# Kernel optimization log

Measured on AMD Instinct MI355X. Metric: run time of the kernel, lower is better.

Reference implementation:

```python
import jax, jax.numpy as jnp
import numpy as np

N = 262144          # particles
E = N * 32          # neighbor pairs (edges)


def wendland(q, h):
    # 2D Wendland C2 kernel, q = r/h in [0,1]
    C = 7.0 / (np.pi) / (h * h)
    b = jnp.clip(1.0 - q, 0.0, None)
    return C * (b ** 4) * (1.0 + 4.0 * q)


def setup_inputs() -> dict:
    key = jax.random.key(0)
    k1, k2, k3, k4, k5 = jax.random.split(key, 5)
    area = jax.random.uniform(k1, (N,), jnp.float32) * 0.5 + 0.5
    density = jax.random.uniform(k2, (N,), jnp.float32) * 0.2 + 0.9
    restDensity = jnp.ones((N,), jnp.float32) * 998.0
    velocity = jax.random.normal(k3, (N, 2), jnp.float32)
    radialDistance = jax.random.uniform(k4, (E,), jnp.float32)
    neighbors = jax.random.randint(k5, (2, E), 0, N, jnp.int64)
    return {
        "fluidCoefficient": jnp.float32(0.01),
        "area": area,
        "density": density,
        "restDensity": restDensity,
        "velocity": velocity,
        "radialDistance": radialDistance,
        "neighbors": neighbors,
        "support": jnp.float32(0.02),
    }


def reference(fluidCoefficient, area, density, restDensity, velocity,
              radialDistance, neighbors, support):
    i = neighbors[0]
    j = neighbors[1]
    fac = fluidCoefficient * restDensity[j] * area[j]           # [E]
    rho_i = density[i] * restDensity[i]                          # [E]
    rho_j = density[j] * restDensity[j]                          # [E]
    v_ij = velocity[j] - velocity[i]                             # [E,2]
    k = wendland(radialDistance, support)                        # [E]
    term = (fac / (rho_i + rho_j) * 2.0 * k)[:, None] * v_ij     # [E,2]
    correction = jax.ops.segment_sum(term, i, num_segments=area.shape[0])
    return correction
```

## Files before the change

### kernel.cpp

```cpp
#include <hip/hip_runtime.h>
#include <math.h>

#ifndef M_PI
#define M_PI 3.14159265358979323846
#endif

#define NBLK  2048
#define CHUNK 4096
#define BSZ   512
#define BSH   9
#define NBK   512

#define SCAN_GB   16
#define SCAN_TH   512
#define SCAN_ROWS (NBLK / SCAN_TH)

__global__ void detect_idx_width(const unsigned* __restrict__ words,
                                 int* __restrict__ flag) {
    if (blockIdx.x == 0 && threadIdx.x == 0) {
        int is64 = 1;
#pragma unroll 1
        for (int k = 1; k < 2048; k += 2) {
            if (words[k] != 0u) { is64 = 0; break; }
        }
        *flag = is64;
    }
}

__global__ __launch_bounds__(256) void precompute_particle(
    const float* __restrict__ fc_p, const float* __restrict__ area,
    const float* __restrict__ density, const float* __restrict__ restDensity,
    const float* __restrict__ velocity, float4* __restrict__ pre, int N)
{
    int p = blockIdx.x * 256 + threadIdx.x;
    if (p >= N) return;
    const float fc = fc_p[0];
    const float rD = restDensity[p];
    const float2 v = ((const float2*)velocity)[p];
    pre[p] = make_float4(fc * rD * area[p], density[p] * rD, v.x, v.y);
}

__global__ __launch_bounds__(256) void pass_count(
    const void* __restrict__ nbr, const int* __restrict__ flag,
    unsigned* __restrict__ table, int E, int chunk, int NBnum)
{
    __shared__ unsigned cnt[NBK];
    for (int t = threadIdx.x; t < NBnum; t += 256) cnt[t] = 0u;
    __syncthreads();
    const int is64 = *flag;
    const long long s = (long long)blockIdx.x * chunk;
    long long e = s + chunk; if (e > E) e = E;
    if (is64) {
        const long long* ni = (const long long*)nbr;
        for (long long idx = s + threadIdx.x; idx < e; idx += 256)
            atomicAdd(&cnt[((int)ni[idx]) >> BSH], 1u);
    } else {
        const int* ni = (const int*)nbr;
        for (long long idx = s + threadIdx.x; idx < e; idx += 256)
            atomicAdd(&cnt[ni[idx] >> BSH], 1u);
    }
    __syncthreads();
    for (int t = threadIdx.x; t < NBnum; t += 256)
        table[(size_t)blockIdx.x * NBnum + t] = cnt[t];
}

__global__ __launch_bounds__(SCAN_TH) void scan_blocks(
    const unsigned* __restrict__ table, unsigned* __restrict__ toff,
    unsigned* __restrict__ btot, int NBnum)
{
    __shared__ unsigned sums[SCAN_TH][SCAN_GB + 1];
    const int t = threadIdx.x;
    const int k0 = blockIdx.x * SCAN_GB;
    unsigned v[SCAN_ROWS][SCAN_GB];
    unsigned loc[SCAN_GB];
#pragma unroll
    for (int g = 0; g < SCAN_GB; ++g) loc[g] = 0u;
#pragma unroll
    for (int r = 0; r < SCAN_ROWS; ++r) {
        const size_t row = (size_t)(t * SCAN_ROWS + r) * NBnum;
#pragma unroll
        for (int g = 0; g < SCAN_GB; ++g) {
            unsigned x = (k0 + g < NBnum) ? table[row + k0 + g] : 0u;
            v[r][g] = x;
            loc[g] += x;
        }
    }
#pragma unroll
    for (int g = 0; g < SCAN_GB; ++g) sums[t][g] = loc[g];
    __syncthreads();
    for (int o = 1; o < SCAN_TH; o <<= 1) {
        unsigned m[SCAN_GB];
#pragma unroll
        for (int g = 0; g < SCAN_GB; ++g) m[g] = (t >= o) ? sums[t - o][g] : 0u;
        __syncthreads();
#pragma unroll
        for (int g = 0; g < SCAN_GB; ++g) sums[t][g] += m[g];
        __syncthreads();
    }
    unsigned pre[SCAN_GB];
#pragma unroll
    for (int g = 0; g < SCAN_GB; ++g) pre[g] = t ? sums[t - 1][g] : 0u;
#pragma unroll
    for (int r = 0; r < SCAN_ROWS; ++r) {
        const size_t row = (size_t)(t * SCAN_ROWS + r) * NBnum;
#pragma unroll
        for (int g = 0; g < SCAN_GB; ++g) {
            if (k0 + g < NBnum) toff[row + k0 + g] = pre[g];
            pre[g] += v[r][g];
        }
    }
    if (t == SCAN_TH - 1) {
#pragma unroll
        for (int g = 0; g < SCAN_GB; ++g)
            if (k0 + g < NBnum) btot[k0 + g] = sums[t][g];
    }
}

__global__ void scan_buckets(const unsigned* __restrict__ btot,
                             unsigned* __restrict__ bstart, int NBnum)
{
    __shared__ unsigned buf[1024];
    const int t = threadIdx.x;
    buf[t] = btot[t];
    __syncthreads();
    for (int o = 1; o < NBnum; o <<= 1) {
        unsigned v = (t >= o) ? buf[t - o] : 0u;
        __syncthreads();
        buf[t] += v;
        __syncthreads();
    }
    bstart[t] = (t == 0) ? 0u : buf[t - 1];
    if (t == NBnum - 1) bstart[NBnum] = buf[t];
}

__global__ __launch_bounds__(256) void pass_scatter(
    const void* __restrict__ nbr, const float* __restrict__ rad,
    const int* __restrict__ flag, const unsigned* __restrict__ table,
    const unsigned* __restrict__ toff, const unsigned* __restrict__ bstart,
    int2* __restrict__ jq, int E, int chunk, int NBnum)
{
    __shared__ int2 buf[CHUNK];
    __shared__ unsigned cur[NBK];
    __shared__ unsigned dst[NBK];

    const int b = blockIdx.x;
    const long long s = (long long)b * chunk;
    long long e = s + chunk; if (e > E) e = E;
    const int n = (int)(e - s);
    if (n <= 0) return;
    const int tid = threadIdx.x;

    for (int k = tid; k < NBnum; k += 256) {
        cur[k] = table[(size_t)b * NBnum + k];
        dst[k] = bstart[k] + toff[(size_t)b * NBnum + k];
    }
    __syncthreads();

    for (int o = 1; o < NBnum; o <<= 1) {
        const int t0 = tid, t1 = tid + 256;
        unsigned v0 = (t0 < NBnum) ? cur[t0] : 0u;
        unsigned m0 = (t0 >= o && t0 < NBnum) ? cur[t0 - o] : 0u;
        unsigned v1 = (t1 < NBnum) ? cur[t1] : 0u;
        unsigned m1 = (t1 >= o && t1 < NBnum) ? cur[t1 - o] : 0u;
        __syncthreads();
        if (t0 < NBnum) cur[t0] = v0 + m0;
        if (t1 < NBnum) cur[t1] = v1 + m1;
        __syncthreads();
    }
    {
        const int t0 = tid, t1 = tid + 256;
        unsigned x0 = (t0 < NBnum) ? (t0 ? cur[t0 - 1] : 0u) : 0u;
        unsigned x1 = (t1 < NBnum) ? cur[t1 - 1] : 0u;
        __syncthreads();
        if (t0 < NBnum) cur[t0] = x0;
        if (t1 < NBnum) cur[t1] = x1;
        __syncthreads();
    }

    const int is64 = *flag;
    if (is64) {
        const long long* ni = (const long long*)nbr;
        const long long* nj = ni + E;
        for (long long idx = s + tid; idx < e; idx += 256) {
            int i = (int)ni[idx];
            int j = (int)nj[idx];
            float q = rad[idx];
            unsigned pos = atomicAdd(&cur[i >> BSH], 1u);
            buf[pos] = make_int2(j | ((i & (BSZ - 1)) << 22),
                                 __float_as_int(q));
        }
    } else {
        const int* ni = (const int*)nbr;
        const int* nj = ni + E;
        for (long long idx = s + tid; idx < e; idx += 256) {
            int i = ni[idx];
            int j = nj[idx];
            float q = rad[idx];
            unsigned pos = atomicAdd(&cur[i >> BSH], 1u);
            buf[pos] = make_int2(j | ((i & (BSZ - 1)) << 22),
                                 __float_as_int(q));
        }
    }
    __syncthreads();

    for (int t = tid; t < n; t += 256) {
        int lo = 0, hi = NBnum - 1;
        while (lo < hi) {
            int mid = (lo + hi) >> 1;
            if (cur[mid] > (unsigned)t) hi = mid; else lo = mid + 1;
        }
        unsigned start = lo ? cur[lo - 1] : 0u;
        jq[dst[lo] + ((unsigned)t - start)] = buf[t];
    }
}

__global__ __launch_bounds__(512) void pass_reduce(
    const int2* __restrict__ jq, const float4* __restrict__ pre,
    const unsigned* __restrict__ bstart, const float* __restrict__ support_p,
    float2* __restrict__ out, int N)
{
    __shared__ float4 plds[BSZ];
    __shared__ float2 acc[BSZ];
    const int k = blockIdx.x;
    const int base = k << BSH;
    const int tid = threadIdx.x;
    {
        int p = base + tid;
        plds[tid] = (p < N) ? pre[p] : make_float4(0.f, 0.f, 0.f, 0.f);
        acc[tid] = make_float2(0.f, 0.f);
    }
    __syncthreads();
    const float h = support_p[0];
    const float C = 7.0f / ((float)M_PI * h * h);
    const unsigned s = bstart[k];
    const unsigned e = bstart[k + 1];
    const unsigned cnt = e - s;
    const unsigned nfull = cnt >> 11;

    for (unsigned r = 0; r < nfull; ++r) {
        const unsigned idx = s + (r << 11) + ((unsigned)tid << 2);
        const int2 pk0 = jq[idx];
        const int2 pk1 = jq[idx + 1];
        const int2 pk2 = jq[idx + 2];
        const int2 pk3 = jq[idx + 3];
        const int j0 = pk0.x & ((1 << 22) - 1), il0 = (pk0.x >> 22) & (BSZ - 1);
        const int j1 = pk1.x & ((1 << 22) - 1), il1 = (pk1.x >> 22) & (BSZ - 1);
        const int j2 = pk2.x & ((1 << 22) - 1), il2 = (pk2.x >> 22) & (BSZ - 1);
        const int j3 = pk3.x & ((1 << 22) - 1), il3 = (pk3.x >> 22) & (BSZ - 1);
        const float4 pj0 = pre[j0];
        const float4 pj1 = pre[j1];
        const float4 pj2 = pre[j2];
        const float4 pj3 = pre[j3];
#define REDUCE_BODY(pj, pk, il)                                              \
        {                                                                    \
            const float q = __int_as_float(pk.y);                            \
            const float4 pi = plds[il];                                      \
            const float b = fmaxf(1.0f - q, 0.0f);                           \
            const float b2 = b * b;                                          \
            const float w = C * (b2 * b2) * fmaf(4.0f, q, 1.0f);             \
            const float sc = pj.x * 2.0f * w / (pi.y + pj.y);                \
            atomicAdd(&acc[il].x, sc * (pj.z - pi.z));                       \
            atomicAdd(&acc[il].y, sc * (pj.w - pi.w));                       \
        }
        REDUCE_BODY(pj0, pk0, il0)
        REDUCE_BODY(pj1, pk1, il1)
        REDUCE_BODY(pj2, pk2, il2)
        REDUCE_BODY(pj3, pk3, il3)
    }
    for (unsigned idx = s + (nfull << 11) + tid; idx < e; idx += 512) {
        const int2 pk = jq[idx];
        const int j = pk.x & ((1 << 22) - 1);
        const int il = (pk.x >> 22) & (BSZ - 1);
        const float4 pj = pre[j];
        REDUCE_BODY(pj, pk, il)
    }
#undef REDUCE_BODY
    __syncthreads();
    {
        int p = base + tid;
        if (p < N) out[p] = acc[tid];
    }
}

__global__ __launch_bounds__(256) void xsph_edge_kernel(
    const float* __restrict__ fc_p, const float* __restrict__ area,
    const float* __restrict__ density, const float* __restrict__ restDensity,
    const float* __restrict__ velocity, const float* __restrict__ rad,
    const void* __restrict__ nbr, const float* __restrict__ support_p,
    const int* __restrict__ flag, float* __restrict__ out, int E)
{
    const int is64 = *flag;
    const float fc = fc_p[0];
    const float h = support_p[0];
    const float C = 7.0f / ((float)M_PI * h * h);
    const long long e0 =
        (long long)(blockIdx.x * (long long)blockDim.x + threadIdx.x) * 4;
    if (e0 >= (long long)E) return;
    int ii[4], jj[4];
    if (is64) {
        const long long* ni = (const long long*)nbr;
        const long long* nj = ni + E;
#pragma unroll
        for (int k = 0; k < 4; ++k) { ii[k] = (int)ni[e0 + k]; jj[k] = (int)nj[e0 + k]; }
    } else {
        const int* ni = (const int*)nbr;
        const int* nj = ni + E;
        int4 iv = *(const int4*)(ni + e0);
        int4 jv = *(const int4*)(nj + e0);
        ii[0] = iv.x; ii[1] = iv.y; ii[2] = iv.z; ii[3] = iv.w;
        jj[0] = jv.x; jj[1] = jv.y; jj[2] = jv.z; jj[3] = jv.w;
    }
    float4 qv = *(const float4*)(rad + e0);
    float qq[4] = {qv.x, qv.y, qv.z, qv.w};
#pragma unroll
    for (int k = 0; k < 4; ++k) {
        const int i = ii[k], j = jj[k];
        const float rDi = restDensity[i], rDj = restDensity[j];
        const float fac = fc * rDj * area[j];
        const float rho_i = density[i] * rDi, rho_j = density[j] * rDj;
        const float2 vi = *(const float2*)(velocity + 2 * i);
        const float2 vj = *(const float2*)(velocity + 2 * j);
        const float q = qq[k];
        const float b = fmaxf(1.0f - q, 0.0f);
        const float b2 = b * b;
        const float w = C * (b2 * b2) * fmaf(4.0f, q, 1.0f);
        const float s = fac * 2.0f * w / (rho_i + rho_j);
        unsafeAtomicAdd(&out[2 * i],     s * (vj.x - vi.x));
        unsafeAtomicAdd(&out[2 * i + 1], s * (vj.y - vi.y));
    }
}

extern "C" void kernel_launch(void* const* d_in, const int* in_sizes, int n_in,
                              void* d_out, int out_size, void* d_ws, size_t ws_size,
                              hipStream_t stream) {
    const float* fc          = (const float*)d_in[0];
    const float* area        = (const float*)d_in[1];
    const float* density     = (const float*)d_in[2];
    const float* restDensity = (const float*)d_in[3];
    const float* velocity    = (const float*)d_in[4];
    const float* rad         = (const float*)d_in[5];
    const void*  nbr         = d_in[6];
    const float* support     = (const float*)d_in[7];

    const int N = in_sizes[1];
    const int E = in_sizes[5];
    const int NBnum = (N + BSZ - 1) / BSZ;
    const int chunk = (int)(((long long)E + NBLK - 1) / NBLK);

    char* ws = (char*)d_ws;
    size_t off = 0;
    int* flag = (int*)(ws + off);               off += 16;
    float4* pre = (float4*)(ws + off);          off += (size_t)N * 16;
    unsigned* table = (unsigned*)(ws + off);    off += (size_t)NBLK * NBnum * 4;
    off = (off + 15) & ~(size_t)15;
    unsigned* toff = (unsigned*)(ws + off);     off += (size_t)NBLK * NBnum * 4;
    off = (off + 15) & ~(size_t)15;
    unsigned* btot = (unsigned*)(ws + off);     off += (size_t)NBnum * 4;
    off = (off + 15) & ~(size_t)15;
    unsigned* bstart = (unsigned*)(ws + off);   off += (size_t)(NBnum + 1) * 4;
    off = (off + 15) & ~(size_t)15;
    int2* jq = (int2*)(ws + off);               off += (size_t)E * 8;
    const size_t need = off;

    detect_idx_width<<<1, 1, 0, stream>>>((const unsigned*)nbr, flag);

    const bool can_sort =
        (ws_size >= need) && (NBnum <= NBK) && (N <= (1 << 22)) &&
        (chunk <= CHUNK) && (E > 0);

    if (can_sort) {
        precompute_particle<<<(N + 255) / 256, 256, 0, stream>>>(
            fc, area, density, restDensity, velocity, pre, N);
        pass_count<<<NBLK, 256, 0, stream>>>(nbr, flag, table, E, chunk, NBnum);
        scan_blocks<<<(NBnum + SCAN_GB - 1) / SCAN_GB, SCAN_TH, 0, stream>>>(
            table, toff, btot, NBnum);
        scan_buckets<<<1, NBnum, 0, stream>>>(btot, bstart, NBnum);
        pass_scatter<<<NBLK, 256, 0, stream>>>(nbr, rad, flag, table, toff,
                                               bstart, jq, E, chunk, NBnum);
        pass_reduce<<<NBnum, 512, 0, stream>>>(jq, pre, bstart, support,
                                               (float2*)d_out, N);
    } else {
        hipMemsetAsync(d_out, 0, (size_t)out_size * sizeof(float), stream);
        const int threads = 256;
        const long long nthreads = ((long long)E + 3) / 4;
        const int blocks = (int)((nthreads + threads - 1) / threads);
        xsph_edge_kernel<<<blocks, threads, 0, stream>>>(
            fc, area, density, restDensity, velocity, rad, nbr, support, flag,
            (float*)d_out, E);
    }
}
```

Before: 230.1 us.

## Split per-bucket reduce across four blocks with partial sums and combine pass

With N=262144 and 512-particle buckets, the reduce pass had only 512 blocks of 512 threads, which underfills the GPU. Each bucket's edge range is now split across four 256-thread blocks. Each block accumulates into its own LDS copy and writes its partial sums to a workspace region reused from the already consumed count tables. A small combine kernel then adds the four partials. This raises parallelism at the cost of an extra launch, extra global traffic for the partials, and each block reloading the bucket's particle data.

After: 233.0 us. Within noise of the previous version (+1.3%).

```diff
diff --git a/kernel.cpp b/kernel.cpp
--- a/kernel.cpp
+++ b/kernel.cpp
@@ -10,6 +10,7 @@
 #define BSZ   512
 #define BSH   9
 #define NBK   512
+#define RSPLIT 4
 
 #define SCAN_GB   16
 #define SCAN_TH   512
@@ -214,31 +215,38 @@
     }
 }
 
-__global__ __launch_bounds__(512) void pass_reduce(
+__global__ __launch_bounds__(256) void pass_reduce(
     const int2* __restrict__ jq, const float4* __restrict__ pre,
     const unsigned* __restrict__ bstart, const float* __restrict__ support_p,
-    float2* __restrict__ out, int N)
+    float2* __restrict__ partial, int N, int pstride)
 {
     __shared__ float4 plds[BSZ];
     __shared__ float2 acc[BSZ];
-    const int k = blockIdx.x;
+    const int blk = blockIdx.x;
+    const int k = blk >> 2;
+    const int r = blk & (RSPLIT - 1);
     const int base = k << BSH;
     const int tid = threadIdx.x;
-    {
-        int p = base + tid;
-        plds[tid] = (p < N) ? pre[p] : make_float4(0.f, 0.f, 0.f, 0.f);
-        acc[tid] = make_float2(0.f, 0.f);
+    for (int t = tid; t < BSZ; t += 256) {
+        int p = base + t;
+        plds[t] = (p < N) ? pre[p] : make_float4(0.f, 0.f, 0.f, 0.f);
+        acc[t] = make_float2(0.f, 0.f);
     }
     __syncthreads();
     const float h = support_p[0];
     const float C = 7.0f / ((float)M_PI * h * h);
-    const unsigned s = bstart[k];
-    const unsigned e = bstart[k + 1];
-    const unsigned cnt = e - s;
-    const unsigned nfull = cnt >> 11;
-
-    for (unsigned r = 0; r < nfull; ++r) {
-        const unsigned idx = s + (r << 11) + ((unsigned)tid << 2);
+    const unsigned s0 = bstart[k];
+    const unsigned cnt = bstart[k + 1] - s0;
+    const unsigned q4 = (cnt + RSPLIT - 1) / RSPLIT;
+    const unsigned soff = min(cnt, (unsigned)r * q4);
+    const unsigned eoff = min(cnt, (unsigned)(r + 1) * q4);
+    const unsigned s = s0 + soff;
+    const unsigned e = s0 + eoff;
+    const unsigned seg = e - s;
+    const unsigned nfull = seg >> 10;
+
+    for (unsigned t4 = 0; t4 < nfull; ++t4) {
+        const unsigned idx = s + (t4 << 10) + ((unsigned)tid << 2);
         const int2 pk0 = jq[idx];
         const int2 pk1 = jq[idx + 1];
         const int2 pk2 = jq[idx + 2];
@@ -267,7 +275,7 @@
         REDUCE_BODY(pj2, pk2, il2)
         REDUCE_BODY(pj3, pk3, il3)
     }
-    for (unsigned idx = s + (nfull << 11) + tid; idx < e; idx += 512) {
+    for (unsigned idx = s + (nfull << 10) + tid; idx < e; idx += 256) {
         const int2 pk = jq[idx];
         const int j = pk.x & ((1 << 22) - 1);
         const int il = (pk.x >> 22) & (BSZ - 1);
@@ -276,10 +284,22 @@
     }
 #undef REDUCE_BODY
     __syncthreads();
-    {
-        int p = base + tid;
-        if (p < N) out[p] = acc[tid];
-    }
+    for (int t = tid; t < BSZ; t += 256)
+        partial[(size_t)r * pstride + base + t] = acc[t];
+}
+
+__global__ __launch_bounds__(256) void pass_combine(
+    const float2* __restrict__ partial, float2* __restrict__ out,
+    int N, int pstride)
+{
+    int p = blockIdx.x * 256 + threadIdx.x;
+    if (p >= N) return;
+    float2 a = partial[p];
+    float2 b = partial[(size_t)pstride + p];
+    float2 c = partial[(size_t)2 * pstride + p];
+    float2 d = partial[(size_t)3 * pstride + p];
+    out[p] = make_float2((a.x + b.x) + (c.x + d.x),
+                         (a.y + b.y) + (c.y + d.y));
 }
 
 __global__ __launch_bounds__(256) void xsph_edge_kernel(
@@ -351,9 +371,11 @@
     size_t off = 0;
     int* flag = (int*)(ws + off);               off += 16;
     float4* pre = (float4*)(ws + off);          off += (size_t)N * 16;
+    size_t table_off = off;
     unsigned* table = (unsigned*)(ws + off);    off += (size_t)NBLK * NBnum * 4;
     off = (off + 15) & ~(size_t)15;
     unsigned* toff = (unsigned*)(ws + off);     off += (size_t)NBLK * NBnum * 4;
+    size_t table_end = off;
     off = (off + 15) & ~(size_t)15;
     unsigned* btot = (unsigned*)(ws + off);     off += (size_t)NBnum * 4;
     off = (off + 15) & ~(size_t)15;
@@ -362,11 +384,16 @@
     int2* jq = (int2*)(ws + off);               off += (size_t)E * 8;
     const size_t need = off;
 
+    float2* partial = (float2*)(ws + table_off);
+    const int pstride = NBnum * BSZ;
+    const bool partial_fits =
+        (size_t)RSPLIT * pstride * 8 <= (table_end - table_off);
+
     detect_idx_width<<<1, 1, 0, stream>>>((const unsigned*)nbr, flag);
 
     const bool can_sort =
         (ws_size >= need) && (NBnum <= NBK) && (N <= (1 << 22)) &&
-        (chunk <= CHUNK) && (E > 0);
+        (chunk <= CHUNK) && (E > 0) && partial_fits;
 
     if (can_sort) {
         precompute_particle<<<(N + 255) / 256, 256, 0, stream>>>(
@@ -377,8 +404,10 @@
         scan_buckets<<<1, NBnum, 0, stream>>>(btot, bstart, NBnum);
         pass_scatter<<<NBLK, 256, 0, stream>>>(nbr, rad, flag, table, toff,
                                                bstart, jq, E, chunk, NBnum);
-        pass_reduce<<<NBnum, 512, 0, stream>>>(jq, pre, bstart, support,
-                                               (float2*)d_out, N);
+        pass_reduce<<<NBnum * RSPLIT, 256, 0, stream>>>(
+            jq, pre, bstart, support, partial, N, pstride);
+        pass_combine<<<(N + 255) / 256, 256, 0, stream>>>(
+            partial, (float2*)d_out, N, pstride);
     } else {
         hipMemsetAsync(d_out, 0, (size_t)out_size * sizeof(float), stream);
         const int threads = 256;
```

## Pack per-particle data to fp16 and split accumulators in reduce pass

Applied to the files above, without the earlier changes.

Per-particle factors and velocities are stored as two half2 values (8 bytes instead of 16), which halves the bytes moved by the random gathers in the reduce pass. Edge records are read with nontemporal loads, the shared accumulators become separate x/y arrays, and the constant 2*C multiply moves out of the inner loop into a new scaling kernel. The cost is an extra kernel launch and a pass over the output, plus fp16 rounding of the density, coefficient and velocity inputs, which may exceed the accuracy tolerance.

New measurement: 234.3 us. About the same (+1.8%).

```diff
diff --git a/kernel.cpp b/kernel.cpp
--- a/kernel.cpp
+++ b/kernel.cpp
@@ -1,4 +1,5 @@
 #include <hip/hip_runtime.h>
+#include <hip/hip_fp16.h>
 #include <math.h>
 
 #ifndef M_PI
@@ -30,14 +31,16 @@
 __global__ __launch_bounds__(256) void precompute_particle(
     const float* __restrict__ fc_p, const float* __restrict__ area,
     const float* __restrict__ density, const float* __restrict__ restDensity,
-    const float* __restrict__ velocity, float4* __restrict__ pre, int N)
+    const float* __restrict__ velocity, uint2* __restrict__ pre, int N)
 {
     int p = blockIdx.x * 256 + threadIdx.x;
     if (p >= N) return;
     const float fc = fc_p[0];
     const float rD = restDensity[p];
     const float2 v = ((const float2*)velocity)[p];
-    pre[p] = make_float4(fc * rD * area[p], density[p] * rD, v.x, v.y);
+    __half2 fr = __floats2half2_rn(fc * rD * area[p], density[p] * rD);
+    __half2 vv = __floats2half2_rn(v.x, v.y);
+    pre[p] = make_uint2(*(unsigned*)&fr, *(unsigned*)&vv);
 }
 
 __global__ __launch_bounds__(256) void pass_count(
@@ -215,23 +218,29 @@
 }
 
 __global__ __launch_bounds__(512) void pass_reduce(
-    const int2* __restrict__ jq, const float4* __restrict__ pre,
-    const unsigned* __restrict__ bstart, const float* __restrict__ support_p,
-    float2* __restrict__ out, int N)
+    const int2* __restrict__ jq, const uint2* __restrict__ pre,
+    const unsigned* __restrict__ bstart, float2* __restrict__ out, int N)
 {
     __shared__ float4 plds[BSZ];
-    __shared__ float2 acc[BSZ];
+    __shared__ float accx[BSZ];
+    __shared__ float accy[BSZ];
     const int k = blockIdx.x;
     const int base = k << BSH;
     const int tid = threadIdx.x;
     {
         int p = base + tid;
-        plds[tid] = (p < N) ? pre[p] : make_float4(0.f, 0.f, 0.f, 0.f);
-        acc[tid] = make_float2(0.f, 0.f);
-    }
-    __syncthreads();
-    const float h = support_p[0];
-    const float C = 7.0f / ((float)M_PI * h * h);
+        if (p < N) {
+            uint2 pv = pre[p];
+            float2 fr = __half22float2(*(__half2*)&pv.x);
+            float2 vv = __half22float2(*(__half2*)&pv.y);
+            plds[tid] = make_float4(fr.x, fr.y, vv.x, vv.y);
+        } else {
+            plds[tid] = make_float4(0.f, 0.f, 0.f, 0.f);
+        }
+        accx[tid] = 0.f;
+        accy[tid] = 0.f;
+    }
+    __syncthreads();
     const unsigned s = bstart[k];
     const unsigned e = bstart[k + 1];
     const unsigned cnt = e - s;
@@ -239,47 +248,64 @@
 
     for (unsigned r = 0; r < nfull; ++r) {
         const unsigned idx = s + (r << 11) + ((unsigned)tid << 2);
-        const int2 pk0 = jq[idx];
-        const int2 pk1 = jq[idx + 1];
-        const int2 pk2 = jq[idx + 2];
-        const int2 pk3 = jq[idx + 3];
-        const int j0 = pk0.x & ((1 << 22) - 1), il0 = (pk0.x >> 22) & (BSZ - 1);
-        const int j1 = pk1.x & ((1 << 22) - 1), il1 = (pk1.x >> 22) & (BSZ - 1);
-        const int j2 = pk2.x & ((1 << 22) - 1), il2 = (pk2.x >> 22) & (BSZ - 1);
-        const int j3 = pk3.x & ((1 << 22) - 1), il3 = (pk3.x >> 22) & (BSZ - 1);
-        const float4 pj0 = pre[j0];
-        const float4 pj1 = pre[j1];
-        const float4 pj2 = pre[j2];
-        const float4 pj3 = pre[j3];
-#define REDUCE_BODY(pj, pk, il)                                              \
+        const long long w0 = __builtin_nontemporal_load((const long long*)(jq + idx));
+        const long long w1 = __builtin_nontemporal_load((const long long*)(jq + idx + 1));
+        const long long w2 = __builtin_nontemporal_load((const long long*)(jq + idx + 2));
+        const long long w3 = __builtin_nontemporal_load((const long long*)(jq + idx + 3));
+        const int x0 = (int)w0, x1 = (int)w1, x2 = (int)w2, x3 = (int)w3;
+        const int j0 = x0 & ((1 << 22) - 1), il0 = (x0 >> 22) & (BSZ - 1);
+        const int j1 = x1 & ((1 << 22) - 1), il1 = (x1 >> 22) & (BSZ - 1);
+        const int j2 = x2 & ((1 << 22) - 1), il2 = (x2 >> 22) & (BSZ - 1);
+        const int j3 = x3 & ((1 << 22) - 1), il3 = (x3 >> 22) & (BSZ - 1);
+        const uint2 g0 = pre[j0];
+        const uint2 g1 = pre[j1];
+        const uint2 g2 = pre[j2];
+        const uint2 g3 = pre[j3];
+#define REDUCE_BODY(gj, qbits, il)                                           \
         {                                                                    \
-            const float q = __int_as_float(pk.y);                            \
+            const float q = __int_as_float((int)(qbits >> 32));              \
+            const float2 fr = __half22float2(*(const __half2*)&gj.x);        \
+            const float2 vv = __half22float2(*(const __half2*)&gj.y);        \
             const float4 pi = plds[il];                                      \
             const float b = fmaxf(1.0f - q, 0.0f);                           \
             const float b2 = b * b;                                          \
-            const float w = C * (b2 * b2) * fmaf(4.0f, q, 1.0f);             \
-            const float sc = pj.x * 2.0f * w / (pi.y + pj.y);                \
-            atomicAdd(&acc[il].x, sc * (pj.z - pi.z));                       \
-            atomicAdd(&acc[il].y, sc * (pj.w - pi.w));                       \
-        }
-        REDUCE_BODY(pj0, pk0, il0)
-        REDUCE_BODY(pj1, pk1, il1)
-        REDUCE_BODY(pj2, pk2, il2)
-        REDUCE_BODY(pj3, pk3, il3)
+            const float w = (b2 * b2) * fmaf(4.0f, q, 1.0f);                 \
+            const float sc = fr.x * w / (pi.y + fr.y);                       \
+            atomicAdd(&accx[il], sc * (vv.x - pi.z));                        \
+            atomicAdd(&accy[il], sc * (vv.y - pi.w));                        \
+        }
+        REDUCE_BODY(g0, w0, il0)
+        REDUCE_BODY(g1, w1, il1)
+        REDUCE_BODY(g2, w2, il2)
+        REDUCE_BODY(g3, w3, il3)
     }
     for (unsigned idx = s + (nfull << 11) + tid; idx < e; idx += 512) {
         const int2 pk = jq[idx];
         const int j = pk.x & ((1 << 22) - 1);
         const int il = (pk.x >> 22) & (BSZ - 1);
-        const float4 pj = pre[j];
-        REDUCE_BODY(pj, pk, il)
+        const uint2 gj = pre[j];
+        const long long qb = ((long long)pk.y) << 32;
+        REDUCE_BODY(gj, qb, il)
     }
 #undef REDUCE_BODY
     __syncthreads();
     {
         int p = base + tid;
-        if (p < N) out[p] = acc[tid];
-    }
+        if (p < N) {
+            out[p] = make_float2(accx[tid], accy[tid]);
+        }
+    }
+}
+
+__global__ __launch_bounds__(256) void pass_scale(
+    float2* __restrict__ out, const float* __restrict__ support_p, int N)
+{
+    int p = blockIdx.x * 256 + threadIdx.x;
+    if (p >= N) return;
+    const float h = support_p[0];
+    const float C = 7.0f / ((float)M_PI * h * h);
+    float2 v = out[p];
+    out[p] = make_float2(v.x * 2.0f * C, v.y * 2.0f * C);
 }
 
 __global__ __launch_bounds__(256) void xsph_edge_kernel(
@@ -350,7 +376,8 @@
     char* ws = (char*)d_ws;
     size_t off = 0;
     int* flag = (int*)(ws + off);               off += 16;
-    float4* pre = (float4*)(ws + off);          off += (size_t)N * 16;
+    uint2* pre = (uint2*)(ws + off);            off += (size_t)N * 8;
+    off = (off + 15) & ~(size_t)15;
     unsigned* table = (unsigned*)(ws + off);    off += (size_t)NBLK * NBnum * 4;
     off = (off + 15) & ~(size_t)15;
     unsigned* toff = (unsigned*)(ws + off);     off += (size_t)NBLK * NBnum * 4;
@@ -377,8 +404,10 @@
         scan_buckets<<<1, NBnum, 0, stream>>>(btot, bstart, NBnum);
         pass_scatter<<<NBLK, 256, 0, stream>>>(nbr, rad, flag, table, toff,
                                                bstart, jq, E, chunk, NBnum);
-        pass_reduce<<<NBnum, 512, 0, stream>>>(jq, pre, bstart, support,
+        pass_reduce<<<NBnum, 512, 0, stream>>>(jq, pre, bstart,
                                                (float2*)d_out, N);
+        pass_scale<<<(N + 255) / 256, 256, 0, stream>>>(
+            (float2*)d_out, support, N);
     } else {
         hipMemsetAsync(d_out, 0, (size_t)out_size * sizeof(float), stream);
         const int threads = 256;
```
